# Kernel tuning notes

Hardware: AMD Instinct MI355X
Metric: run time of the kernel (lower is better)

The kernel has to match this reference:

```python
import jax, jax.numpy as jnp
import numpy as np

B, S, D = 2, 2048, 2048          # batch, seq_len, model_dim
H, HD, RD, L = 16, 128, 64, 512  # heads, head_dim, rope_dim, latent_dim


def _rope_cos_sin(seq_len, dim, dtype):
    inv_freq = 1.0 / (10000.0 ** (jnp.arange(0, dim, 2, dtype=jnp.float32) / dim))
    freqs = jnp.outer(jnp.arange(seq_len, dtype=jnp.float32), inv_freq)  # [S, dim/2]
    emb = jnp.concatenate([freqs, freqs], axis=-1)                        # [S, dim]
    return jnp.cos(emb).astype(dtype), jnp.sin(emb).astype(dtype)


def _rotate_half(x):
    x1, x2 = jnp.split(x, 2, axis=-1)
    return jnp.concatenate([-x2, x1], axis=-1)


def _apply_rope(q, k):
    # q, k: [B, S, H, rope_dim]
    cos, sin = _rope_cos_sin(q.shape[1], q.shape[-1], q.dtype)
    cos = cos[None, :, None, :]
    sin = sin[None, :, None, :]
    return q * cos + _rotate_half(q) * sin, k * cos + _rotate_half(k) * sin


def setup_inputs() -> dict:
    key = jax.random.key(0)
    ks = jax.random.split(key, 6)
    x = jax.random.normal(ks[0], (B, S, D), dtype=jnp.float32)
    mask = jnp.tril(jnp.ones((1, 1, S, S), dtype=jnp.bool_))  # causal
    s = lambda fan_in: 1.0 / np.sqrt(fan_in)
    w_kv_down = jax.random.normal(ks[1], (D, L), jnp.float32) * s(D)
    w_kv_up = jax.random.normal(ks[2], (L, H * (2 * HD + RD)), jnp.float32) * s(L)
    w_q_down = jax.random.normal(ks[3], (D, L), jnp.float32) * s(D)
    w_q_up = jax.random.normal(ks[4], (L, H * (HD + RD)), jnp.float32) * s(L)
    w_o = jax.random.normal(ks[5], (H * HD, D), jnp.float32) * s(H * HD)
    return dict(x=x, mask=mask, w_kv_down=w_kv_down, w_kv_up=w_kv_up,
                w_q_down=w_q_down, w_q_up=w_q_up, w_o=w_o)


def reference(x, mask, w_kv_down, w_kv_up, w_q_down, w_q_up, w_o):
    b, s, _ = x.shape
    # low-rank KV path
    kv_full = (x @ w_kv_down @ w_kv_up).reshape(b, s, H, 2 * HD + RD)
    k_content = kv_full[..., :HD]
    k_rope = kv_full[..., HD:HD + RD]
    v = kv_full[..., HD + RD:]                     # [b, s, H, HD]
    # low-rank Q path
    q_full = (x @ w_q_down @ w_q_up).reshape(b, s, H, HD + RD)
    q_content = q_full[..., :HD]
    q_rope = q_full[..., HD:]
    # partial RoPE on the rope slice only
    q_rope, k_rope = _apply_rope(q_rope, k_rope)
    q = jnp.concatenate([q_content, q_rope], axis=-1)  # [b, s, H, HD+RD]
    k = jnp.concatenate([k_content, k_rope], axis=-1)
    scale = 1.0 / np.sqrt(HD + RD)
    scores = jnp.einsum('bqhd,bkhd->bhqk', q, k) * scale
    scores = jnp.where(mask, scores, jnp.finfo(scores.dtype).min)
    attn = jax.nn.softmax(scores, axis=-1)          # dropout_p=0.0 -> identity
    context = jnp.einsum('bhqk,bkhd->bqhd', attn, v).reshape(b, s, H * HD)
    return context @ w_o
```

## Files before the change

kernel.cpp:

```cpp
#include <hip/hip_runtime.h>
#include <hip/hip_bf16.h>

#define B_ 2
#define S_ 2048
#define D_ 2048
#define H_ 16
#define HD_ 128
#define RD_ 64
#define L_ 512
#define BS_ (B_ * S_)
#define KVH 320
#define QH 192

typedef unsigned short u16;
typedef __bf16 bf16x8 __attribute__((ext_vector_type(8)));
typedef float f32x4 __attribute__((ext_vector_type(4)));
typedef float f32x16 __attribute__((ext_vector_type(16)));
typedef unsigned short us8 __attribute__((ext_vector_type(8)));
typedef unsigned short us4 __attribute__((ext_vector_type(4)));

#define MFMA16(A, B, C) __builtin_amdgcn_mfma_f32_16x16x32_bf16((A), (B), (C), 0, 0, 0)
#define MFMA32(A, B, C) __builtin_amdgcn_mfma_f32_32x32x16_bf16((A), (B), (C), 0, 0, 0)

__device__ __forceinline__ u16 f2bf(float f) {
    unsigned int u = __builtin_bit_cast(unsigned int, f);
    u += 0x7FFFu + ((u >> 16) & 1u);
    return (u16)(u >> 16);
}
__device__ __forceinline__ float bf2f(u16 u) {
    unsigned int x = ((unsigned int)u) << 16;
    return __builtin_bit_cast(float, x);
}
__device__ __forceinline__ void async16(const void* g, void* l) {
    __builtin_amdgcn_global_load_lds((void __attribute__((address_space(1)))*)g,
                                     (void __attribute__((address_space(3)))*)l, 16, 0, 0);
}
__device__ __forceinline__ int swz4(int row) { return (row + (row >> 2)) & 3; }
__device__ __forceinline__ unsigned int cvtpk_bf16(float lo, float hi) {
    unsigned int r;
    asm("v_cvt_pk_bf16_f32 %0, %1, %2" : "=v"(r) : "v"(lo), "v"(hi));
    return r;
}

__global__ __launch_bounds__(256) void conv_f32_bf16(const float* __restrict__ in,
                                                     u16* __restrict__ outp) {
    const int i = blockIdx.x * 256 + threadIdx.x;
    float4 v = *(const float4*)(in + (size_t)i * 4);
    us4 o; o[0] = f2bf(v.x); o[1] = f2bf(v.y); o[2] = f2bf(v.z); o[3] = f2bf(v.w);
    *(us4*)(outp + (size_t)i * 4) = o;
}

__global__ __launch_bounds__(256) void transpose_f32_bf16(const float* __restrict__ W,
                                                          u16* __restrict__ Wt,
                                                          int K, int N) {
    __shared__ float tile[32][33];
    const int t = threadIdx.x, tx = t & 31, ty = t >> 5;
    const int n0 = blockIdx.x * 32, k0 = blockIdx.y * 32;
#pragma unroll
    for (int r = 0; r < 4; r++)
        tile[ty + 8 * r][tx] = W[(size_t)(k0 + ty + 8 * r) * N + n0 + tx];
    __syncthreads();
#pragma unroll
    for (int r = 0; r < 4; r++)
        Wt[(size_t)(n0 + ty + 8 * r) * K + k0 + tx] = f2bf(tile[tx][ty + 8 * r]);
}

__global__ __launch_bounds__(256) void transpose_v(const u16* __restrict__ kvf,
                                                   u16* __restrict__ vtg) {
    __shared__ u16 tile[64][72];
    const int t = threadIdx.x;
    const int r = t >> 2, cb = (t & 3) * 16;
    const int bh = blockIdx.z, b = bh >> 4, h = bh & 15;
    const int s0 = blockIdx.x * 64, d0 = blockIdx.y * 64;

    const u16* src = kvf + (size_t)(b * S_ + s0 + r) * (H_ * KVH) + h * KVH + QH + d0 + cb;
    *(us8*)&tile[r][cb]     = *(const us8*)(src);
    *(us8*)&tile[r][cb + 8] = *(const us8*)(src + 8);
    __syncthreads();

    u16 tmp[16];
#pragma unroll
    for (int j = 0; j < 16; j++) tmp[j] = tile[cb + j][r];
    u16* dst = vtg + ((size_t)bh * HD_ + d0 + r) * S_ + s0 + cb;
    *(us8*)(dst)     = *(us8*)&tmp[0];
    *(us8*)(dst + 8) = *(us8*)&tmp[8];
}

__global__ __launch_bounds__(256) void rope_table(float* __restrict__ cs) {
    const int idx = blockIdx.x * 256 + threadIdx.x;
    const int d = idx & 31, s = idx >> 5;
    const float inv_freq = powf(10000.0f, -(float)d * (1.0f / 32.0f));
    const float ang = (float)s * inv_freq;
    cs[s * 64 + d]      = cosf(ang);
    cs[s * 64 + 32 + d] = sinf(ang);
}

__global__ __launch_bounds__(256) void rope_both(u16* __restrict__ qf,
                                                 u16* __restrict__ kvf,
                                                 const float* __restrict__ cs) {
    const int idx = blockIdx.x * 256 + threadIdx.x;
    const int d = idx & 31;
    const int h = (idx >> 5) & (H_ - 1);
    const int s = (idx >> 9) & (S_ - 1);
    const int b = idx >> 20;
    const int stride = blockIdx.y ? KVH : QH;
    u16* buf = blockIdx.y ? kvf : qf;

    const float c  = cs[s * 64 + d];
    const float sn = cs[s * 64 + 32 + d];

    u16* p = buf + ((size_t)((b * S_ + s) * H_) + h) * stride + HD_ + d;
    const float x1 = bf2f(p[0]);
    const float x2 = bf2f(p[32]);
    p[0]  = f2bf(x1 * c - x2 * sn);
    p[32] = f2bf(x2 * c + x1 * sn);
}

template <int WM, int WN, int TM, int TN, bool OUT_F32>
__global__ __launch_bounds__(WM * WN * 64) void gemm_bf16(
    const u16* __restrict__ A, int lda,
    const u16* __restrict__ Bt, int ldb,
    void* __restrict__ Cv, int ldc, int K, float alpha) {
    constexpr int BMt = WM * TM * 16;
    constexpr int BNt = WN * TN * 16;
    constexpr int NW  = WM * WN;
    constexpr int CA  = BMt / 16;
    constexpr int CB  = BNt / 16;

    __shared__ u16 As[BMt * 32];
    __shared__ u16 Bs[BNt * 32];

    const int t = threadIdx.x, w = t >> 6, l = t & 63;
    const int quad = l >> 4, n16 = l & 15;
    const int wr = w / WN, wc = w % WN;
    const size_t m0 = (size_t)blockIdx.y * BMt;
    const size_t n0 = (size_t)blockIdx.x * BNt;
    const int rowc = l >> 2, sbp = l & 3;

    f32x4 acc[TM][TN];
#pragma unroll
    for (int i = 0; i < TM; i++)
#pragma unroll
        for (int j = 0; j < TN; j++) acc[i][j] = (f32x4){0.f, 0.f, 0.f, 0.f};

    for (int k0 = 0; k0 < K; k0 += 32) {
#pragma unroll
        for (int c = w; c < CA; c += NW) {
            const int row = c * 16 + rowc;
            const int colc = ((sbp - swz4(row)) & 3) * 8;
            async16(A + (m0 + row) * lda + k0 + colc, &As[c * 512 + l * 8]);
        }
#pragma unroll
        for (int c = w; c < CB; c += NW) {
            const int row = c * 16 + rowc;
            const int colc = ((sbp - swz4(row)) & 3) * 8;
            async16(Bt + (n0 + row) * ldb + k0 + colc, &Bs[c * 512 + l * 8]);
        }
        __syncthreads();

        bf16x8 af[TM], bfr[TN];
#pragma unroll
        for (int i = 0; i < TM; i++) {
            const int row = wr * TM * 16 + i * 16 + n16;
            af[i] = *(const bf16x8*)&As[row * 32 + ((quad + swz4(row)) & 3) * 8];
        }
#pragma unroll
        for (int j = 0; j < TN; j++) {
            const int row = wc * TN * 16 + j * 16 + n16;
            bfr[j] = *(const bf16x8*)&Bs[row * 32 + ((quad + swz4(row)) & 3) * 8];
        }
#pragma unroll
        for (int i = 0; i < TM; i++)
#pragma unroll
            for (int j = 0; j < TN; j++) acc[i][j] = MFMA16(af[i], bfr[j], acc[i][j]);
        __syncthreads();
    }

#pragma unroll
    for (int i = 0; i < TM; i++) {
#pragma unroll
        for (int j = 0; j < TN; j++) {
#pragma unroll
            for (int r = 0; r < 4; r++) {
                const size_t row = m0 + wr * TM * 16 + i * 16 + quad * 4 + r;
                const size_t col = n0 + wc * TN * 16 + j * 16 + n16;
                const float v = acc[i][j][r] * alpha;
                if (OUT_F32) ((float*)Cv)[row * ldc + col] = v;
                else         ((u16*)Cv)[row * ldc + col] = f2bf(v);
            }
        }
    }
}

__global__ __launch_bounds__(256, 2) void attn_mfma(const u16* __restrict__ qf,
                                                    const u16* __restrict__ kvf,
                                                    const u16* __restrict__ vtg,
                                                    u16* __restrict__ ctx) {
    __shared__ u16 Ks[2][3 * 64 * 64];
    __shared__ u16 Vs[128 * 64];

    const int t = threadIdx.x, w = t >> 6, lane = t & 63;
    const int l31 = lane & 31, hi = lane >> 5;

    const int wg = blockIdx.x;
    const int xcd = wg & 7, ii = wg >> 3;
    const int tt = ii & 15;
    const int pp = (tt & 1) ? (tt >> 1) : (15 - (tt >> 1));
    const int qi = (ii & 32) ? (15 - pp) : pp;
    const int bh = xcd + 8 * (ii >> 4);
    const int b = bh >> 4, h = bh & 15;
    const int Q0 = qi * 128;

    const u16* Kbase = kvf + (size_t)(b * S_) * (H_ * KVH) + h * KVH;
    const u16* Vbase = vtg + (size_t)bh * HD_ * S_;

    const int scol = ((lane & 7) ^ (lane >> 3)) * 8;
    const int krl  = lane >> 3;

    bf16x8 qfrag[12];
    {
        const u16* qr = qf + (size_t)(b * S_ + Q0 + w * 32 + l31) * (H_ * QH) + h * QH + hi * 8;
#pragma unroll
        for (int c = 0; c < 12; c++) qfrag[c] = *(const bf16x8*)(qr + c * 16);
    }
    asm volatile("" ::: "memory");

    f32x16 O[4];
#pragma unroll
    for (int i = 0; i < 4; i++)
#pragma unroll
        for (int r = 0; r < 16; r++) O[i][r] = 0.f;
    float lrun = 0.f;

    const int qg = Q0 + w * 32 + l31;
    const int qmaxw = Q0 + w * 32 + 31;
    const int nkt = Q0 / 64 + 2;

#define ISSUE_K(KT, BUF)                                                        \
    _Pragma("unroll")                                                           \
    for (int ch = w; ch < 24; ch += 4) {                                        \
        const int c3 = ch >> 3, kq = ch & 7;                                    \
        async16(Kbase + (size_t)((KT) * 64 + kq * 8 + krl) * (H_ * KVH)         \
                      + c3 * 64 + scol,                                         \
                &Ks[BUF][c3 * 4096 + kq * 512 + lane * 8]);                     \
    }
#define ISSUE_V(KT)                                                             \
    _Pragma("unroll")                                                           \
    for (int ch = w; ch < 16; ch += 4) {                                        \
        async16(Vbase + (size_t)(ch * 8 + krl) * S_ + (KT) * 64 + scol,         \
                &Vs[ch * 512 + lane * 8]);                                      \
    }

    ISSUE_K(0, 0);
    ISSUE_V(0);

    for (int kt = 0; kt < nkt; kt++) {
        const int cur = kt & 1;
        if (kt > 0) {
            asm volatile("s_barrier" ::: "memory");
            ISSUE_V(kt);
        }
        if (kt + 1 < nkt) {
            ISSUE_K(kt + 1, cur ^ 1);
            asm volatile("s_waitcnt vmcnt(10)" ::: "memory");
        } else {
            asm volatile("s_waitcnt vmcnt(4)" ::: "memory");
        }
        asm volatile("s_barrier" ::: "memory");

        const bool active = (kt * 64) <= qmaxw;
        bf16x8 pfrag[4];
        if (active) {
            const int swz = (l31 & 7) * 8;
            f32x16 sA, sB;
#pragma unroll
            for (int r = 0; r < 16; r++) { sA[r] = 0.f; sB[r] = 0.f; }
            __builtin_amdgcn_s_setprio(1);
#pragma unroll
            for (int c = 0; c < 12; c++) {
                const int cb = (c & 3) * 16 + hi * 8;
                const int base = (c >> 2) * 4096 + (cb ^ swz);
                bf16x8 kf0 = *(const bf16x8*)&Ks[cur][base + l31 * 64];
                bf16x8 kf1 = *(const bf16x8*)&Ks[cur][base + (32 + l31) * 64];
                sA = MFMA32(kf0, qfrag[c], sA);
                sB = MFMA32(kf1, qfrag[c], sB);
            }
            __builtin_amdgcn_s_setprio(0);

            const bool diag = (kt * 64 + 63) > (Q0 + w * 32);
#pragma unroll
            for (int r = 0; r < 16; r++) {
                const int crow = (r & 3) + 8 * (r >> 2) + 4 * hi;
                float pa = exp2f(sA[r]);
                float pb = exp2f(sB[r]);
                if (diag) {
                    if (kt * 64 + crow > qg) pa = 0.f;
                    if (kt * 64 + 32 + crow > qg) pb = 0.f;
                }
                lrun += pa + pb;
                sA[r] = pa;
                sB[r] = pb;
            }

#pragma unroll
            for (int s = 0; s < 4; s++) {
                const f32x16 src = (s < 2) ? sA : sB;
                const int r0 = (s & 1) * 8;
                unsigned int x0 = cvtpk_bf16(src[r0 + 0], src[r0 + 1]);
                unsigned int y0 = cvtpk_bf16(src[r0 + 4], src[r0 + 5]);
                unsigned int x1 = cvtpk_bf16(src[r0 + 2], src[r0 + 3]);
                unsigned int y1 = cvtpk_bf16(src[r0 + 6], src[r0 + 7]);
                asm volatile("v_permlane32_swap_b32 %0, %1" : "+v"(x0), "+v"(y0));
                asm volatile("v_permlane32_swap_b32 %0, %1" : "+v"(x1), "+v"(y1));
                union { unsigned int wv[4]; bf16x8 v; } u;
                u.wv[0] = x0; u.wv[1] = x1; u.wv[2] = y0; u.wv[3] = y1;
                pfrag[s] = u.v;
            }
        }

        if (kt + 1 < nkt) asm volatile("s_waitcnt vmcnt(6)" ::: "memory");
        else              asm volatile("s_waitcnt vmcnt(0)" ::: "memory");
        asm volatile("s_barrier" ::: "memory");

        if (active) {
            __builtin_amdgcn_s_setprio(1);
#pragma unroll
            for (int s = 0; s < 4; s++) {
#pragma unroll
                for (int dt = 0; dt < 4; dt++) {
                    const int d = dt * 32 + l31;
                    bf16x8 vf = *(const bf16x8*)&Vs[d * 64 + ((s * 16 + hi * 8) ^ ((d & 7) * 8))];
                    O[dt] = MFMA32(pfrag[s], vf, O[dt]);
                }
            }
            __builtin_amdgcn_s_setprio(0);
        }
    }
#undef ISSUE_K
#undef ISSUE_V

    lrun += __shfl_xor(lrun, 32, 64);
    float inv[16];
#pragma unroll
    for (int r = 0; r < 16; r++) {
        const int crow = (r & 3) + 8 * (r >> 2) + 4 * hi;
        inv[r] = 1.0f / __shfl(lrun, crow, 64);
    }
#pragma unroll
    for (int dt = 0; dt < 4; dt++)
#pragma unroll
        for (int r = 0; r < 16; r++) {
            const int crow = (r & 3) + 8 * (r >> 2) + 4 * hi;
            const int qrow = Q0 + w * 32 + crow;
            ctx[(size_t)(b * S_ + qrow) * (H_ * HD_) + h * HD_ + dt * 32 + l31] =
                f2bf(O[dt][r] * inv[r]);
        }
}

extern "C" void kernel_launch(void* const* d_in, const int* in_sizes, int n_in,
                              void* d_out, int out_size, void* d_ws, size_t ws_size,
                              hipStream_t stream) {
    const float* x         = (const float*)d_in[0];
    const float* w_kv_down = (const float*)d_in[2];
    const float* w_kv_up   = (const float*)d_in[3];
    const float* w_q_down  = (const float*)d_in[4];
    const float* w_q_up    = (const float*)d_in[5];
    const float* w_o       = (const float*)d_in[6];
    float* out = (float*)d_out;

    char* ws = (char*)d_ws;
    size_t off = 0;
    u16* xb      = (u16*)(ws + off); off += (size_t)BS_ * D_ * 2;
    u16* wdt     = (u16*)(ws + off); off += (size_t)1024 * D_ * 2;
    u16* wkvup_t = (u16*)(ws + off); off += (size_t)(H_ * KVH) * L_ * 2;
    u16* wqup_t  = (u16*)(ws + off); off += (size_t)(H_ * QH) * L_ * 2;
    u16* wo_t    = (u16*)(ws + off); off += (size_t)D_ * (H_ * HD_) * 2;
    u16* low     = (u16*)(ws + off); off += (size_t)BS_ * 1024 * 2;
    u16* kv_full = (u16*)(ws + off); off += (size_t)BS_ * H_ * KVH * 2;
    u16* q_full  = (u16*)(ws + off); off += (size_t)BS_ * H_ * QH * 2;
    u16* vtg     = (u16*)(ws + off); off += (size_t)B_ * H_ * HD_ * S_ * 2;
    u16* ctx     = (u16*)(ws + off); off += (size_t)BS_ * H_ * HD_ * 2;
    float* ropecs = (float*)(ws + off); off += (size_t)S_ * 64 * 4;

    const float qscale = 1.442695041f / 13.856406461f;

    rope_table<<<256, 256, 0, stream>>>(ropecs);
    conv_f32_bf16<<<(BS_ * D_) / 1024, 256, 0, stream>>>(x, xb);
    transpose_f32_bf16<<<dim3(L_ / 32, D_ / 32), 256, 0, stream>>>(w_kv_down, wdt, D_, L_);
    transpose_f32_bf16<<<dim3(L_ / 32, D_ / 32), 256, 0, stream>>>(w_q_down, wdt + (size_t)512 * D_, D_, L_);
    transpose_f32_bf16<<<dim3((H_ * KVH) / 32, L_ / 32), 256, 0, stream>>>(w_kv_up, wkvup_t, L_, H_ * KVH);
    transpose_f32_bf16<<<dim3((H_ * QH) / 32, L_ / 32), 256, 0, stream>>>(w_q_up, wqup_t, L_, H_ * QH);
    transpose_f32_bf16<<<dim3(D_ / 32, (H_ * HD_) / 32), 256, 0, stream>>>(w_o, wo_t, H_ * HD_, D_);

    gemm_bf16<2, 2, 4, 2, false><<<dim3(1024 / 64, BS_ / 128), 256, 0, stream>>>(
        xb, D_, wdt, D_, low, 1024, D_, 1.0f);
    gemm_bf16<2, 2, 4, 4, false><<<dim3((H_ * KVH) / 128, BS_ / 128), 256, 0, stream>>>(
        low, 1024, wkvup_t, L_, kv_full, H_ * KVH, L_, 1.0f);
    gemm_bf16<2, 2, 4, 4, false><<<dim3((H_ * QH) / 128, BS_ / 128), 256, 0, stream>>>(
        low + 512, 1024, wqup_t, L_, q_full, H_ * QH, L_, qscale);

    rope_both<<<dim3((B_ * S_ * H_ * 32) / 256, 2), 256, 0, stream>>>(q_full, kv_full, ropecs);

    transpose_v<<<dim3(S_ / 64, HD_ / 64, B_ * H_), 256, 0, stream>>>(kv_full, vtg);

    attn_mfma<<<dim3(512), 256, 0, stream>>>(q_full, kv_full, vtg, ctx);

    gemm_bf16<2, 2, 4, 4, true><<<dim3(D_ / 128, BS_ / 128), 256, 0, stream>>>(
        ctx, D_, wo_t, D_, out, D_, D_, 1.0f);
}
```

Measured before the change: 390.4 us.

## Replace GEMM with 128x256 double-buffered, K64, XCD-aware tiled kernel

Replaces the templated single-buffered GEMM with a fixed 128x256 tile kernel using 8 waves, a 64-wide K step, and double-buffered LDS so the next tile's global-to-LDS loads overlap the current MFMAs. Block IDs are remapped so that row blocks are grouped by XCD, which should improve L2 reuse of the A operand. The larger tile raises data reuse per load, at the cost of more LDS and registers and fewer blocks for the smaller GEMMs (the 1024-wide one launches only 128 blocks).

```diff
diff --git a/kernel.cpp b/kernel.cpp
--- a/kernel.cpp
+++ b/kernel.cpp
@@ -35,7 +35,6 @@
     __builtin_amdgcn_global_load_lds((void __attribute__((address_space(1)))*)g,
                                      (void __attribute__((address_space(3)))*)l, 16, 0, 0);
 }
-__device__ __forceinline__ int swz4(int row) { return (row + (row >> 2)) & 3; }
 __device__ __forceinline__ unsigned int cvtpk_bf16(float lo, float hi) {
     unsigned int r;
     asm("v_cvt_pk_bf16_f32 %0, %1, %2" : "=v"(r) : "v"(lo), "v"(hi));
@@ -116,74 +115,85 @@
     p[32] = f2bf(x2 * c + x1 * sn);
 }
 
-template <int WM, int WN, int TM, int TN, bool OUT_F32>
-__global__ __launch_bounds__(WM * WN * 64) void gemm_bf16(
+template <bool OUT_F32>
+__global__ __launch_bounds__(512, 2) void gemm256(
     const u16* __restrict__ A, int lda,
     const u16* __restrict__ Bt, int ldb,
     void* __restrict__ Cv, int ldc, int K, float alpha) {
-    constexpr int BMt = WM * TM * 16;
-    constexpr int BNt = WN * TN * 16;
-    constexpr int NW  = WM * WN;
-    constexpr int CA  = BMt / 16;
-    constexpr int CB  = BNt / 16;
-
-    __shared__ u16 As[BMt * 32];
-    __shared__ u16 Bs[BNt * 32];
-
-    const int t = threadIdx.x, w = t >> 6, l = t & 63;
-    const int quad = l >> 4, n16 = l & 15;
-    const int wr = w / WN, wc = w % WN;
-    const size_t m0 = (size_t)blockIdx.y * BMt;
-    const size_t n0 = (size_t)blockIdx.x * BNt;
-    const int rowc = l >> 2, sbp = l & 3;
-
-    f32x4 acc[TM][TN];
-#pragma unroll
-    for (int i = 0; i < TM; i++)
-#pragma unroll
-        for (int j = 0; j < TN; j++) acc[i][j] = (f32x4){0.f, 0.f, 0.f, 0.f};
-
-    for (int k0 = 0; k0 < K; k0 += 32) {
-#pragma unroll
-        for (int c = w; c < CA; c += NW) {
-            const int row = c * 16 + rowc;
-            const int colc = ((sbp - swz4(row)) & 3) * 8;
-            async16(A + (m0 + row) * lda + k0 + colc, &As[c * 512 + l * 8]);
-        }
-#pragma unroll
-        for (int c = w; c < CB; c += NW) {
-            const int row = c * 16 + rowc;
-            const int colc = ((sbp - swz4(row)) & 3) * 8;
-            async16(Bt + (n0 + row) * ldb + k0 + colc, &Bs[c * 512 + l * 8]);
-        }
-        __syncthreads();
-
-        bf16x8 af[TM], bfr[TN];
-#pragma unroll
-        for (int i = 0; i < TM; i++) {
-            const int row = wr * TM * 16 + i * 16 + n16;
-            af[i] = *(const bf16x8*)&As[row * 32 + ((quad + swz4(row)) & 3) * 8];
-        }
-#pragma unroll
-        for (int j = 0; j < TN; j++) {
-            const int row = wc * TN * 16 + j * 16 + n16;
-            bfr[j] = *(const bf16x8*)&Bs[row * 32 + ((quad + swz4(row)) & 3) * 8];
-        }
-#pragma unroll
-        for (int i = 0; i < TM; i++)
-#pragma unroll
-            for (int j = 0; j < TN; j++) acc[i][j] = MFMA16(af[i], bfr[j], acc[i][j]);
-        __syncthreads();
-    }
-
-#pragma unroll
-    for (int i = 0; i < TM; i++) {
-#pragma unroll
-        for (int j = 0; j < TN; j++) {
+    __shared__ u16 As[2][128 * 64];
+    __shared__ u16 Bs[2][256 * 64];
+
+    const int t = threadIdx.x, w = t >> 6, lane = t & 63;
+    const int quad = lane >> 4, n16 = lane & 15;
+    const int wr = w >> 2, wc = w & 3;
+
+    const int wg = blockIdx.x;
+    const int xcd = wg & 7, ysub = (wg >> 3) & 3, xblk = wg >> 5;
+    const size_t m0 = (size_t)((xcd << 2) | ysub) * 128;
+    const size_t n0 = (size_t)xblk * 256;
+
+    const int dg   = ((((lane & 7) - (lane >> 3)) & 7)) * 8;
+    const int srow = lane >> 3;
+    const int posA0 = ((quad + (n16 & 7)) & 7) * 8;
+    const int posA1 = ((quad + 4 + (n16 & 7)) & 7) * 8;
+
+    f32x4 acc[4][4];
+#pragma unroll
+    for (int i = 0; i < 4; i++)
+#pragma unroll
+        for (int j = 0; j < 4; j++) acc[i][j] = (f32x4){0.f, 0.f, 0.f, 0.f};
+
+#define STG(K0, BUF)                                                          \
+    _Pragma("unroll")                                                         \
+    for (int i_ = 0; i_ < 2; i_++) {                                          \
+        const int c_ = w + 8 * i_;                                            \
+        async16(A + (m0 + c_ * 8 + srow) * lda + (K0) + dg,                   \
+                &As[BUF][c_ * 512 + lane * 8]);                               \
+    }                                                                         \
+    _Pragma("unroll")                                                         \
+    for (int i_ = 0; i_ < 4; i_++) {                                          \
+        const int c_ = w + 8 * i_;                                            \
+        async16(Bt + (n0 + c_ * 8 + srow) * ldb + (K0) + dg,                  \
+                &Bs[BUF][c_ * 512 + lane * 8]);                               \
+    }
+
+    STG(0, 0)
+
+    const int NT = K / 64;
+    for (int tt = 0; tt < NT; tt++) {
+        const int cur = tt & 1;
+        asm volatile("s_waitcnt vmcnt(0)" ::: "memory");
+        asm volatile("s_barrier" ::: "memory");
+        bf16x8 bfr[4][2];
+#pragma unroll
+        for (int j = 0; j < 4; j++) {
+            const int br = (wc * 64 + j * 16 + n16) * 64;
+            bfr[j][0] = *(const bf16x8*)&Bs[cur][br + posA0];
+            bfr[j][1] = *(const bf16x8*)&Bs[cur][br + posA1];
+        }
+        if (tt + 1 < NT) { STG((tt + 1) * 64, cur ^ 1) }
+#pragma unroll
+        for (int i = 0; i < 4; i++) {
+            const int ar = (wr * 64 + i * 16 + n16) * 64;
+            bf16x8 a0 = *(const bf16x8*)&As[cur][ar + posA0];
+            bf16x8 a1 = *(const bf16x8*)&As[cur][ar + posA1];
+#pragma unroll
+            for (int j = 0; j < 4; j++) {
+                acc[i][j] = MFMA16(a0, bfr[j][0], acc[i][j]);
+                acc[i][j] = MFMA16(a1, bfr[j][1], acc[i][j]);
+            }
+        }
+    }
+#undef STG
+
+#pragma unroll
+    for (int i = 0; i < 4; i++) {
+#pragma unroll
+        for (int j = 0; j < 4; j++) {
 #pragma unroll
             for (int r = 0; r < 4; r++) {
-                const size_t row = m0 + wr * TM * 16 + i * 16 + quad * 4 + r;
-                const size_t col = n0 + wc * TN * 16 + j * 16 + n16;
+                const size_t row = m0 + wr * 64 + i * 16 + quad * 4 + r;
+                const size_t col = n0 + wc * 64 + j * 16 + n16;
                 const float v = acc[i][j][r] * alpha;
                 if (OUT_F32) ((float*)Cv)[row * ldc + col] = v;
                 else         ((u16*)Cv)[row * ldc + col] = f2bf(v);
@@ -392,11 +402,11 @@
     transpose_f32_bf16<<<dim3((H_ * QH) / 32, L_ / 32), 256, 0, stream>>>(w_q_up, wqup_t, L_, H_ * QH);
     transpose_f32_bf16<<<dim3(D_ / 32, (H_ * HD_) / 32), 256, 0, stream>>>(w_o, wo_t, H_ * HD_, D_);
 
-    gemm_bf16<2, 2, 4, 2, false><<<dim3(1024 / 64, BS_ / 128), 256, 0, stream>>>(
+    gemm256<false><<<dim3(32 * (1024 / 256)), 512, 0, stream>>>(
         xb, D_, wdt, D_, low, 1024, D_, 1.0f);
-    gemm_bf16<2, 2, 4, 4, false><<<dim3((H_ * KVH) / 128, BS_ / 128), 256, 0, stream>>>(
+    gemm256<false><<<dim3(32 * ((H_ * KVH) / 256)), 512, 0, stream>>>(
         low, 1024, wkvup_t, L_, kv_full, H_ * KVH, L_, 1.0f);
-    gemm_bf16<2, 2, 4, 4, false><<<dim3((H_ * QH) / 128, BS_ / 128), 256, 0, stream>>>(
+    gemm256<false><<<dim3(32 * ((H_ * QH) / 256)), 512, 0, stream>>>(
         low + 512, 1024, wqup_t, L_, q_full, H_ * QH, L_, qscale);
 
     rope_both<<<dim3((B_ * S_ * H_ * 32) / 256, 2), 256, 0, stream>>>(q_full, kv_full, ropecs);
@@ -405,6 +415,6 @@
 
     attn_mfma<<<dim3(512), 256, 0, stream>>>(q_full, kv_full, vtg, ctx);
 
-    gemm_bf16<2, 2, 4, 4, true><<<dim3(D_ / 128, BS_ / 128), 256, 0, stream>>>(
+    gemm256<true><<<dim3(32 * (D_ / 256)), 512, 0, stream>>>(
         ctx, D_, wo_t, D_, out, D_, D_, 1.0f);
 }
```

Result: no change. 382.8 us (-1.9%).
